# Optimization experiments

Measured on AMD Instinct MI355X. Metric: run time of the kernel, lower is better.

## Reference

```python
import jax, jax.numpy as jnp
import numpy as np

EPS = 1e-6

def _ln(x, g, b):
    mu = x.mean(-1, keepdims=True)
    var = ((x - mu) ** 2).mean(-1, keepdims=True)
    return (x - mu) * jax.lax.rsqrt(var + EPS) * g + b

def _ln_l2_grad(z, target, g, b):
    # grad of 0.5*||LN(z)*g+b - target||^2 wrt z (fused L2/LayerNorm backward used by TTT)
    d = z.shape[-1]
    mu = z.mean(-1, keepdims=True)
    var = ((z - mu) ** 2).mean(-1, keepdims=True)
    std = jnp.sqrt(var + EPS)
    zh = (z - mu) / std
    go = (zh * g + b) - target
    gxh = go * g
    return (d * gxh - gxh.sum(-1, keepdims=True) - zh * (gxh * zh).sum(-1, keepdims=True)) / (d * std)

def _forward(x, W_down, b_down, Wq, Wk, Wv, Wo, W1, b1, ttt_g, ttt_b,
             lr_w, lr_b, post_g, post_b, norm_g, norm_b, W_up, b_up):
    B, S, D = x.shape
    A = W_down.shape[1]
    H, hd, _ = W1.shape
    # adapter down projection + SiLU
    h = jax.nn.silu(x @ W_down + b_down)                      # [B,S,A]
    # TTT-Linear: q/k/v projections split into heads
    xq = (h @ Wq).reshape(B, S, H, hd)
    xk = (h @ Wk).reshape(B, S, H, hd)
    xv = (h @ Wv).reshape(B, S, H, hd)
    eta = jax.nn.sigmoid(h @ lr_w + lr_b) / hd                # [B,S,H] token-wise learnable inner lr (base_lr=1)
    W1_0 = jnp.broadcast_to(W1, (B, H, hd, hd))
    b1_0 = jnp.broadcast_to(b1, (B, H, 1, hd))
    xs = (xq.transpose(1, 0, 2, 3), xk.transpose(1, 0, 2, 3),
          xv.transpose(1, 0, 2, 3), eta.transpose(1, 0, 2))

    def step(carry, ins):
        W, bb = carry                                         # [B,H,hd,hd], [B,H,1,hd]
        q, k, v, e = ins                                      # [B,H,hd] x3, [B,H]
        Z = jnp.einsum('bhd,bhde->bhe', k, W) + bb[:, :, 0, :]
        g = _ln_l2_grad(Z, v - k, ttt_g, ttt_b)               # inner-loop grad wrt pre-LN activations
        e4 = e[:, :, None, None]
        Wn = W - e4 * (k[..., :, None] * g[..., None, :])     # fast-weight SGD update
        bn = bb - e4 * g[:, :, None, :]
        Zq = jnp.einsum('bhd,bhde->bhe', q, Wn) + bn[:, :, 0, :]
        out = q + _ln(Zq, ttt_g, ttt_b)                       # per-head TTT post residual
        return (Wn, bn), out

    _, ys = jax.lax.scan(step, (W1_0, b1_0), xs)              # ys: [S,B,H,hd]
    t = ys.transpose(1, 0, 2, 3).reshape(B, S, A)
    t = _ln(t, post_g, post_b) @ Wo                           # TTT post-norm + output projection
    out = _ln(t, norm_g, norm_b)                              # adapter LayerNorm
    return out @ W_up + b_up                                  # adapter up projection (residual unused in source)

def setup_inputs() -> dict:
    key = jax.random.key(0)
    ks = jax.random.split(key, 12)
    B, S, D, A, H = 4, 1024, 768, 192, 3
    hd = A // H
    s = 0.02
    return {
        'x': jax.random.normal(ks[0], (B, S, D), jnp.float32),
        'W_down': jax.random.normal(ks[1], (D, A), jnp.float32) * s,
        'b_down': jnp.zeros((A,), jnp.float32),
        'Wq': jax.random.normal(ks[2], (A, A), jnp.float32) * s,
        'Wk': jax.random.normal(ks[3], (A, A), jnp.float32) * s,
        'Wv': jax.random.normal(ks[4], (A, A), jnp.float32) * s,
        'Wo': jax.random.normal(ks[5], (A, A), jnp.float32) * s,
        'W1': jax.random.normal(ks[6], (H, hd, hd), jnp.float32) * s,
        'b1': jnp.zeros((H, 1, hd), jnp.float32),
        'ttt_g': jnp.ones((H, hd), jnp.float32),
        'ttt_b': jnp.zeros((H, hd), jnp.float32),
        'lr_w': jax.random.normal(ks[7], (A, H), jnp.float32) * s,
        'lr_b': jnp.zeros((H,), jnp.float32),
        'post_g': jnp.ones((A,), jnp.float32),
        'post_b': jnp.zeros((A,), jnp.float32),
        'norm_g': jnp.ones((A,), jnp.float32),
        'norm_b': jnp.zeros((A,), jnp.float32),
        'W_up': jax.random.normal(ks[8], (A, D), jnp.float32) * s,
        'b_up': jnp.zeros((D,), jnp.float32),
    }

def reference(x, W_down, b_down, Wq, Wk, Wv, Wo, W1, b1, ttt_g, ttt_b,
              lr_w, lr_b, post_g, post_b, norm_g, norm_b, W_up, b_up):
    return _forward(x, W_down, b_down, Wq, Wk, Wv, Wo, W1, b1, ttt_g, ttt_b,
                    lr_w, lr_b, post_g, post_b, norm_g, norm_b, W_up, b_up)
```

## Files before the change

### kernel.cpp

```cpp
#include <hip/hip_runtime.h>
#include <hip/hip_bf16.h>
#include <math.h>

#define BDIM 4
#define SDIM 1024
#define DDIM 768
#define ADIM 192
#define HDIM 3
#define HD   64
#define MROWS (BDIM*SDIM)
#define NCHUNK (SDIM/32)
#define EPSLN 1e-6f

template<int CTRL, int RMASK, bool BC>
__device__ __forceinline__ float dpp_add_step(float x) {
    int t = __builtin_amdgcn_update_dpp(0, __float_as_int(x), CTRL, RMASK, 0xf, BC);
    return x + __int_as_float(t);
}
__device__ __forceinline__ float wave_bcast_sum(float x) {
    x = dpp_add_step<0x111, 0xf, true >(x);
    x = dpp_add_step<0x112, 0xf, true >(x);
    x = dpp_add_step<0x114, 0xf, true >(x);
    x = dpp_add_step<0x118, 0xf, true >(x);
    x = dpp_add_step<0x142, 0xa, false>(x);
    x = dpp_add_step<0x143, 0xc, false>(x);
    return __int_as_float(__builtin_amdgcn_readlane(__float_as_int(x), 63));
}
__device__ __forceinline__ float rl(float v, int lane) {
    return __int_as_float(__builtin_amdgcn_readlane(__float_as_int(v), lane));
}
__device__ __forceinline__ float fast_rsq(float x) {
    float r;
    asm("v_rsq_f32 %0, %1" : "=v"(r) : "v"(x));
    return r;
}
__device__ __forceinline__ void red5_asm(float& a, float& b, float& c,
                                         float& d, float& e) {
#define R5_SHR(N)                                                              \
    asm("v_add_f32 %0, %0, %0 row_shr:" #N " row_mask:0xf bank_mask:0xf bound_ctrl:0" : "+v"(a)); \
    asm("v_add_f32 %0, %0, %0 row_shr:" #N " row_mask:0xf bank_mask:0xf bound_ctrl:0" : "+v"(b)); \
    asm("v_add_f32 %0, %0, %0 row_shr:" #N " row_mask:0xf bank_mask:0xf bound_ctrl:0" : "+v"(c)); \
    asm("v_add_f32 %0, %0, %0 row_shr:" #N " row_mask:0xf bank_mask:0xf bound_ctrl:0" : "+v"(d)); \
    asm("v_add_f32 %0, %0, %0 row_shr:" #N " row_mask:0xf bank_mask:0xf bound_ctrl:0" : "+v"(e));
#define R5_BC(N, RM)                                                           \
    asm("v_add_f32 %0, %0, %0 row_bcast:" #N " row_mask:" #RM " bank_mask:0xf" : "+v"(a)); \
    asm("v_add_f32 %0, %0, %0 row_bcast:" #N " row_mask:" #RM " bank_mask:0xf" : "+v"(b)); \
    asm("v_add_f32 %0, %0, %0 row_bcast:" #N " row_mask:" #RM " bank_mask:0xf" : "+v"(c)); \
    asm("v_add_f32 %0, %0, %0 row_bcast:" #N " row_mask:" #RM " bank_mask:0xf" : "+v"(d)); \
    asm("v_add_f32 %0, %0, %0 row_bcast:" #N " row_mask:" #RM " bank_mask:0xf" : "+v"(e));
    R5_SHR(1) R5_SHR(2) R5_SHR(4) R5_SHR(8)
    R5_BC(15, 0xa) R5_BC(31, 0xc)
#undef R5_SHR
#undef R5_BC
}

__global__ __launch_bounds__(64) void lnstats(
    const float* __restrict__ in, float2* __restrict__ st)
{
    int row = blockIdx.x, tid = threadIdx.x;
    float x0 = in[(size_t)row * ADIM + tid];
    float x1 = in[(size_t)row * ADIM + 64 + tid];
    float x2 = in[(size_t)row * ADIM + 128 + tid];
    float s1 = wave_bcast_sum((x0 + x1) + x2);
    float s2 = wave_bcast_sum(fmaf(x0, x0, fmaf(x1, x1, x2 * x2)));
    if (tid == 0) {
        float mu = s1 * (1.f / 192.f);
        float var = s2 * (1.f / 192.f) - mu * mu;
        st[row] = make_float2(mu, rsqrtf(var + EPSLN));
    }
}

template<int ACT, int LAYOUT, int LNA>
__global__ __launch_bounds__(256) void gemm_k(
    const float* __restrict__ A, const float* __restrict__ Bm,
    const float* __restrict__ bias, float* __restrict__ C,
    int M, int N, int K,
    const float2* __restrict__ lnst, const float* __restrict__ lng,
    const float* __restrict__ lnbb)
{
    __shared__ float As[16][68];
    __shared__ float Bs[16][68];
    const int tid = threadIdx.x;
    const int bm = blockIdx.y * 64, bn = blockIdx.x * 64;
    const int tr = tid >> 4, tc = tid & 15;
    float acc[4][4] = {};

    for (int k0 = 0; k0 < K; k0 += 16) {
        #pragma unroll
        for (int p = 0; p < 4; ++p) {
            int m = (tid >> 4) + p * 16;
            int kk = tid & 15;
            float av = A[(size_t)(bm + m) * K + k0 + kk];
            if (LNA) {
                float2 stv = lnst[bm + m];
                av = fmaf((av - stv.x) * stv.y, lng[k0 + kk], lnbb[k0 + kk]);
            }
            As[kk][m] = av;
        }
        #pragma unroll
        for (int p = 0; p < 4; ++p) {
            int kk = (tid >> 6) + p * 4;
            int n = tid & 63;
            Bs[kk][n] = Bm[(size_t)(k0 + kk) * N + bn + n];
        }
        __syncthreads();
        #pragma unroll
        for (int kk = 0; kk < 16; ++kk) {
            const float4 a4 = *(const float4*)&As[kk][tr * 4];
            const float4 b4 = *(const float4*)&Bs[kk][tc * 4];
            float aa[4] = {a4.x, a4.y, a4.z, a4.w};
            float bb[4] = {b4.x, b4.y, b4.z, b4.w};
            #pragma unroll
            for (int i = 0; i < 4; ++i)
                #pragma unroll
                for (int j = 0; j < 4; ++j)
                    acc[i][j] = fmaf(aa[i], bb[j], acc[i][j]);
        }
        __syncthreads();
    }

    #pragma unroll
    for (int i = 0; i < 4; ++i) {
        int m = bm + tr * 4 + i;
        #pragma unroll
        for (int j = 0; j < 4; ++j) {
            int n = bn + tc * 4 + j;
            float v = acc[i][j];
            if (bias) v += bias[n];
            if (ACT == 1) v = v / (1.f + __expf(-v));
            if (LAYOUT == 0) {
                C[(size_t)m * N + n] = v;
            } else {
                int b  = m >> 10, s = m & 1023;
                int hh = n >> 6,  d = n & 63;
                C[(((size_t)b * HDIM + hh) * SDIM + s) * HD + d] = v;
            }
        }
    }
}

__global__ __launch_bounds__(256) void gemm_qkv(
    const float* __restrict__ A, const float* __restrict__ BWq,
    const float* __restrict__ BWk, const float* __restrict__ BWv,
    float* __restrict__ Cbase)
{
    const float* Bm = (blockIdx.z == 0) ? BWq : (blockIdx.z == 1) ? BWk : BWv;
    float* C = Cbase + (size_t)blockIdx.z * ((size_t)MROWS * ADIM);
    __shared__ float As[16][68];
    __shared__ float Bs[16][68];
    const int tid = threadIdx.x;
    const int bm = blockIdx.y * 64, bn = blockIdx.x * 64;
    const int tr = tid >> 4, tc = tid & 15;
    float acc[4][4] = {};

    for (int k0 = 0; k0 < ADIM; k0 += 16) {
        #pragma unroll
        for (int p = 0; p < 4; ++p) {
            int m = (tid >> 4) + p * 16;
            int kk = tid & 15;
            As[kk][m] = A[(size_t)(bm + m) * ADIM + k0 + kk];
        }
        #pragma unroll
        for (int p = 0; p < 4; ++p) {
            int kk = (tid >> 6) + p * 4;
            int n = tid & 63;
            Bs[kk][n] = Bm[(size_t)(k0 + kk) * ADIM + bn + n];
        }
        __syncthreads();
        #pragma unroll
        for (int kk = 0; kk < 16; ++kk) {
            const float4 a4 = *(const float4*)&As[kk][tr * 4];
            const float4 b4 = *(const float4*)&Bs[kk][tc * 4];
            float aa[4] = {a4.x, a4.y, a4.z, a4.w};
            float bb[4] = {b4.x, b4.y, b4.z, b4.w};
            #pragma unroll
            for (int i = 0; i < 4; ++i)
                #pragma unroll
                for (int j = 0; j < 4; ++j)
                    acc[i][j] = fmaf(aa[i], bb[j], acc[i][j]);
        }
        __syncthreads();
    }

    #pragma unroll
    for (int i = 0; i < 4; ++i) {
        int m = bm + tr * 4 + i;
        #pragma unroll
        for (int j = 0; j < 4; ++j) {
            int n = bn + tc * 4 + j;
            int b  = m >> 10, s = m & 1023;
            int hh = n >> 6,  d = n & 63;
            C[(((size_t)b * HDIM + hh) * SDIM + s) * HD + d] = acc[i][j];
        }
    }
}

__global__ __launch_bounds__(192) void eta_kernel(
    const float* __restrict__ h, const float* __restrict__ lr_w,
    const float* __restrict__ lr_b, float* __restrict__ etab)
{
    const int row = blockIdx.x, tid = threadIdx.x, wave = tid >> 6;
    __shared__ float part[3][3];
    float hv = h[(size_t)row * ADIM + tid];
    float p0 = hv * lr_w[tid * 3 + 0];
    float p1 = hv * lr_w[tid * 3 + 1];
    float p2 = hv * lr_w[tid * 3 + 2];
    float s0 = wave_bcast_sum(p0);
    float s1 = wave_bcast_sum(p1);
    float s2 = wave_bcast_sum(p2);
    if ((tid & 63) == 0) {
        part[wave][0] = s0; part[wave][1] = s1; part[wave][2] = s2;
    }
    __syncthreads();
    if (tid < 3) {
        float acc = (part[0][tid] + part[1][tid]) + part[2][tid] + lr_b[tid];
        float e = 1.f / (1.f + __expf(-acc)) * (1.f / 64.f);
        int b = row >> 10, s = row & 1023;
        etab[((size_t)(b * HDIM + tid)) * SDIM + s] = e;
    }
}

__global__ __launch_bounds__(256) void ab_kernel(
    const float* __restrict__ qb, const float* __restrict__ kb,
    float* __restrict__ vb,
    const float* __restrict__ ttt_g, const float* __restrict__ ttt_b,
    float* __restrict__ Ab, float* __restrict__ Bb,
    float* __restrict__ r6b)
{
    int bh = blockIdx.x >> 5, c = blockIdx.x & 31, cs = c * 32;
    int hh = bh % HDIM;
    __shared__ float Kc[32][65], Qc[32][65], Vc[32][65];
    for (int i = threadIdx.x; i < 2048; i += 256) {
        int t = i >> 6, j = i & 63;
        Kc[t][j] = kb[((size_t)bh * SDIM + cs + t) * HD + j];
        Qc[t][j] = qb[((size_t)bh * SDIM + cs + t) * HD + j];
        Vc[t][j] = vb[((size_t)bh * SDIM + cs + t) * HD + j];
    }
    __syncthreads();
    size_t base = ((size_t)(bh * NCHUNK + c)) * 1024;
    for (int e = threadIdx.x; e < 1024; e += 256) {
        int t = e >> 5, s = e & 31;
        float a = 1.f, b = 1.f;
        #pragma unroll
        for (int j = 0; j < 64; ++j) {
            float ks = Kc[s][j];
            a = fmaf(Kc[t][j], ks, a);
            b = fmaf(Qc[t][j], ks, b);
        }
        Ab[base + e] = a;
        Bb[base + e] = b;
    }
    for (int i = threadIdx.x; i < 2048; i += 256) {
        int t = i >> 6, j = i & 63;
        float gwv = ttt_g[hh * 64 + j], bwv = ttt_b[hh * 64 + j];
        float av = fmaf(-(Vc[t][j] - Kc[t][j]), gwv, bwv * gwv);
        Vc[t][j] = av;
        vb[((size_t)bh * SDIM + cs + t) * HD + j] = av;
    }
    __syncthreads();
    if (threadIdx.x < 32) {
        int t = threadIdx.x;
        float acc = 0.f;
        #pragma unroll
        for (int j = 0; j < 64; ++j) acc += Vc[t][j];
        r6b[(size_t)bh * SDIM + cs + t] = acc;
    }
}

__device__ __forceinline__ void stage_chunk(
    int pp, int cc, int bh, int idx, int nth,
    const float* __restrict__ kbuf, const float* __restrict__ abuf,
    const float* __restrict__ Ab, const float* __restrict__ etab,
    const float* __restrict__ r6b,
    float4* K4, float4* a4, float4* A4, float2* er6)
{
    const float4* kg = (const float4*)(kbuf + ((size_t)bh * SDIM + cc * 32) * HD);
    const float4* ag = (const float4*)(abuf + ((size_t)bh * SDIM + cc * 32) * HD);
    const float4* Ag = (const float4*)(Ab + ((size_t)(bh * NCHUNK + cc)) * 1024);
    for (int i = idx; i < 512; i += nth) K4[pp * 512 + i] = kg[i];
    for (int i = idx; i < 512; i += nth) a4[pp * 512 + i] = ag[i];
    for (int i = idx; i < 256; i += nth) A4[pp * 256 + i] = Ag[i];
    for (int i = idx; i < 32; i += nth)
        er6[pp * 32 + i] = make_float2(
            etab[(size_t)bh * SDIM + cc * 32 + i] * (1.f / 64.f),
            r6b[(size_t)bh * SDIM + cc * 32 + i]);
}

__global__ __launch_bounds__(256, 1) void ttt_scan(
    const float* __restrict__ kbuf, const float* __restrict__ abuf,
    const float* __restrict__ etab, const float* __restrict__ Ab,
    const float* __restrict__ r6b,
    const float* __restrict__ W1,   const float* __restrict__ b1,
    const float* __restrict__ ttt_g, const float* __restrict__ ttt_b,
    float* __restrict__ Gbuf, float* __restrict__ W0save, float* __restrict__ b0save)
{
    const int bh = blockIdx.x, hh = bh % HDIM;
    const int tid = threadIdx.x, lane = tid & 63;
    const int wv = tid >> 6;
    __shared__ float  Zp[4][16][64];
    __shared__ float4 K4s[2 * 512];
    __shared__ float4 a4s[2 * 512];
    __shared__ float4 A4s[2 * 256];
    __shared__ float2 er6s[2 * 32];
    __shared__ float  Gl[16][64];

    float Wreg[16];
    #pragma unroll
    for (int r = 0; r < 16; ++r)
        Wreg[r] = W1[hh * 4096 + (wv * 16 + r) * 64 + lane];
    float breg = b1[hh * 64 + lane];
    const float gw = ttt_g[hh * 64 + lane];
    const float bw = ttt_b[hh * 64 + lane];
    const float w3 = gw * gw;
    (void)bw;
    const float Cg2 = wave_bcast_sum(w3);
    const float* a_f = (const float*)a4s;

    stage_chunk(0, 0, bh, tid, 256, kbuf, abuf, Ab, etab, r6b,
                K4s, a4s, A4s, er6s);
    __syncthreads();

    for (int c = 0; c < NCHUNK; ++c) {
        const int cs = c * 32;
        const int p = c & 1;

        {
            float* Wd = W0save + ((size_t)(bh * NCHUNK + c)) * 4096
                        + (wv * 16) * 64 + lane;
            #pragma unroll
            for (int r = 0; r < 16; ++r) Wd[r * 64] = Wreg[r];
            if (tid < 64) b0save[(bh * NCHUNK + c) * 64 + tid] = breg;
        }

        #pragma unroll
        for (int h = 0; h < 2; ++h) {
            const int h16 = h * 16, h4 = h * 4;

            float Zt[16];
            #pragma unroll
            for (int i = 0; i < 16; ++i) {
                const int t = h16 + i;
                float zt = 0.f;
                #pragma unroll
                for (int r4 = 0; r4 < 4; ++r4) {
                    const float4 kv = K4s[p * 512 + t * 16 + wv * 4 + r4];
                    zt = fmaf(kv.x, Wreg[r4 * 4 + 0], zt);
                    zt = fmaf(kv.y, Wreg[r4 * 4 + 1], zt);
                    zt = fmaf(kv.z, Wreg[r4 * 4 + 2], zt);
                    zt = fmaf(kv.w, Wreg[r4 * 4 + 3], zt);
                }
                Zt[i] = zt;
            }
            if (wv != 0) {
                #pragma unroll
                for (int i = 0; i < 16; ++i) Zp[wv][i][lane] = Zt[i];
            }
            __syncthreads();

            if (wv == 0) {
                float Z[16];
                #pragma unroll
                for (int i = 0; i < 16; ++i) {
                    float q1 = Zp[1][i][lane], q2 = Zp[2][i][lane],
                          q3 = Zp[3][i][lane];
                    Z[i] = ((Zt[i] + q1) + (q2 + q3)) + breg;
                }
                float4 avA[4], avB[4];
                float aA, aB; float2 erA, erB;
                #pragma unroll
                for (int q = 0; q < 4; ++q)
                    avA[q] = A4s[p * 256 + h16 * 8 + h4 + q];
                aA  = a_f[p * 2048 + h16 * 64 + lane];
                erA = er6s[p * 32 + h16];
#define TOK(I, avC, aC, erC, avN, aN, erN)                                     \
    {                                                                          \
        if ((I) < 15) {                                                        \
            _Pragma("unroll")                                                  \
            for (int q = 0; q < 4; ++q)                                        \
                avN[q] = A4s[p * 256 + (h16 + (I) + 1) * 8 + h4 + q];          \
            aN  = a_f[p * 2048 + (h16 + (I) + 1) * 64 + lane];                 \
            erN = er6s[p * 32 + h16 + (I) + 1];                                \
        }                                                                      \
        float z  = Z[I];                                                       \
        float a  = aC;                                                         \
        float zg = z * w3;                                                     \
        float x1 = z, x2 = z * z, x3 = zg, x4 = zg * z, x5 = z * a;            \
        red5_asm(x1, x2, x3, x4, x5);                                          \
        float r1 = rl(x1, 63), r2 = rl(x2, 63), r3 = rl(x3, 63);               \
        float r4 = rl(x4, 63), r5 = rl(x5, 63);                                \
        float r6t = (erC).y;                                                   \
        float mu   = r1 * (1.f / 64.f);                                        \
        float var  = fmaf(-mu, mu, r2 * (1.f / 64.f));                         \
        float rstd = fast_rsq(var + EPSLN);                                    \
        float mc   = mu * Cg2;                                                 \
        float sgxh = fmaf(rstd, r3 - mc, r6t);                                 \
        float t4v  = fmaf(mu, mc, fmaf(-2.f * mu, r3, r4));                    \
        float sgz  = fmaf(rstd * rstd, t4v, rstd * (r5 - mu * r6t));           \
        float zh   = (z - mu) * rstd;                                          \
        float gxh  = fmaf(zh, w3, a);                                          \
        float ge   = (fmaf(64.f, gxh, -sgxh) - zh * sgz) * (rstd * (erC).x);   \
        Gl[I][lane] = ge;                                                      \
        _Pragma("unroll")                                                      \
        for (int u = (I) + 1; u < 16; ++u) {                                   \
            const float4 c4 = avC[(u) >> 2]; const int m4 = (u) & 3;           \
            float Atu = (m4 == 0) ? c4.x : (m4 == 1) ? c4.y                    \
                      : (m4 == 2) ? c4.z : c4.w;                               \
            Z[u] = fmaf(-Atu, ge, Z[u]);                                       \
        }                                                                      \
    }
                #pragma unroll
                for (int tp = 0; tp < 8; ++tp) {
                    TOK(2 * tp,     avA, aA, erA, avB, aB, erB)
                    TOK(2 * tp + 1, avB, aB, erB, avA, aA, erA)
                }
#undef TOK
            } else if (h == 0 && c < NCHUNK - 1) {
                stage_chunk(p ^ 1, c + 1, bh, tid - 64, 192,
                            kbuf, abuf, Ab, etab, r6b, K4s, a4s, A4s, er6s);
            }
            __syncthreads();

            float btot = 0.f;
            #pragma unroll
            for (int s = 0; s < 16; ++s) {
                float gd = Gl[s][lane];
                btot += gd;
                #pragma unroll
                for (int r4 = 0; r4 < 4; ++r4) {
                    const float4 kv = K4s[p * 512 + (h16 + s) * 16 + wv * 4 + r4];
                    Wreg[r4 * 4 + 0] = fmaf(-kv.x, gd, Wreg[r4 * 4 + 0]);
                    Wreg[r4 * 4 + 1] = fmaf(-kv.y, gd, Wreg[r4 * 4 + 1]);
                    Wreg[r4 * 4 + 2] = fmaf(-kv.z, gd, Wreg[r4 * 4 + 2]);
                    Wreg[r4 * 4 + 3] = fmaf(-kv.w, gd, Wreg[r4 * 4 + 3]);
                }
            }
            breg -= btot;
            {
                float* gb = Gbuf + ((size_t)bh * SDIM + cs + h16) * HD + lane;
                #pragma unroll
                for (int r = 0; r < 4; ++r)
                    gb[(wv * 4 + r) * HD] = Gl[wv * 4 + r][lane];
            }
        }
    }
}

__global__ __launch_bounds__(256) void post_kernel(
    const float* __restrict__ qbuf, const float* __restrict__ Bb,
    const float* __restrict__ Gbuf, const float* __restrict__ W0save,
    const float* __restrict__ b0save,
    const float* __restrict__ ttt_g, const float* __restrict__ ttt_b,
    float* __restrict__ ys)
{
    const int bh = blockIdx.x >> 5, c = blockIdx.x & 31, cs = c * 32;
    const int b = bh / HDIM, hh = bh % HDIM;
    const int tid = threadIdx.x, lane = tid & 63, wave = tid >> 6;
    __shared__ float Qc[32][65];
    __shared__ float W0l[64][65];
    __shared__ float Gl[32][64];
    for (int i = tid; i < 2048; i += 256) {
        int t = i >> 6, j = i & 63;
        Qc[t][j] = qbuf[((size_t)bh * SDIM + cs + t) * HD + j];
        Gl[t][j] = Gbuf[((size_t)bh * SDIM + cs + t) * HD + j];
    }
    for (int i = tid; i < 4096; i += 256)
        W0l[i >> 6][i & 63] = W0save[((size_t)(bh * NCHUNK + c)) * 4096 + i];
    __syncthreads();

    const float bb0 = b0save[(bh * NCHUNK + c) * 64 + lane];
    const float gw = ttt_g[hh * 64 + lane], bw = ttt_b[hh * 64 + lane];
    float acc[8];
    #pragma unroll
    for (int r = 0; r < 8; ++r) acc[r] = bb0;
    for (int j = 0; j < 64; ++j) {
        float w0 = W0l[j][lane];
        #pragma unroll
        for (int r = 0; r < 8; ++r)
            acc[r] = fmaf(Qc[wave * 8 + r][j], w0, acc[r]);
    }
    float Breg[8];
    size_t bbase = ((size_t)(bh * NCHUNK + c)) * 1024;
    #pragma unroll
    for (int r = 0; r < 8; ++r)
        Breg[r] = Bb[bbase + (wave * 8 + r) * 32 + (lane & 31)];
    #pragma unroll
    for (int s = 0; s < 32; ++s) {
        float gd = Gl[s][lane];
        #pragma unroll
        for (int r = 0; r < 8; ++r) {
            int t = wave * 8 + r;
            float Bts = rl(Breg[r], s);
            acc[r] = (s <= t) ? fmaf(-Bts, gd, acc[r]) : acc[r];
        }
    }
    #pragma unroll
    for (int r = 0; r < 8; ++r) {
        int t = wave * 8 + r;
        float s1 = wave_bcast_sum(acc[r]);
        float s2 = wave_bcast_sum(acc[r] * acc[r]);
        float mu = s1 * (1.f / 64.f);
        float var = s2 * (1.f / 64.f) - mu * mu;
        float rstd = rsqrtf(var + EPSLN);
        float zh = (acc[r] - mu) * rstd;
        float val = zh * gw + bw + Qc[t][lane];
        ys[((size_t)(b * SDIM) + cs + t) * ADIM + hh * HD + lane] = val;
    }
}

extern "C" void kernel_launch(void* const* d_in, const int* in_sizes, int n_in,
                              void* d_out, int out_size, void* d_ws, size_t ws_size,
                              hipStream_t stream)
{
    const float* x      = (const float*)d_in[0];
    const float* W_down = (const float*)d_in[1];
    const float* b_down = (const float*)d_in[2];
    const float* Wq     = (const float*)d_in[3];
    const float* Wk     = (const float*)d_in[4];
    const float* Wv     = (const float*)d_in[5];
    const float* Wo     = (const float*)d_in[6];
    const float* W1     = (const float*)d_in[7];
    const float* b1     = (const float*)d_in[8];
    const float* ttt_g  = (const float*)d_in[9];
    const float* ttt_b  = (const float*)d_in[10];
    const float* lr_w   = (const float*)d_in[11];
    const float* lr_b   = (const float*)d_in[12];
    const float* post_g = (const float*)d_in[13];
    const float* post_b = (const float*)d_in[14];
    const float* norm_g = (const float*)d_in[15];
    const float* norm_b = (const float*)d_in[16];
    const float* W_up   = (const float*)d_in[17];
    const float* b_up   = (const float*)d_in[18];
    float* out = (float*)d_out;

    float* ws = (float*)d_ws;
    const size_t SZ = (size_t)MROWS * ADIM;
    float* h    = ws;
    float* qb   = ws + SZ;
    float* kb   = ws + 2 * SZ;
    float* vb   = ws + 3 * SZ;
    float* Gb   = ws + 4 * SZ;
    float* etab = ws + 5 * SZ;
    float* Ab   = etab + 12288;
    float* Bb   = Ab + 393216;
    float* W0s  = Bb + 393216;
    float* b0s  = W0s + 1572864;
    float* r6b  = b0s + 24576;
    float2* lnst = (float2*)(r6b + 12288);
    float* ysb  = h;
    float* tbuf = qb;

    gemm_k<1, 0, 0><<<dim3(ADIM / 64, MROWS / 64), 256, 0, stream>>>(
        x, W_down, b_down, h, MROWS, ADIM, DDIM, nullptr, nullptr, nullptr);
    gemm_qkv<<<dim3(ADIM / 64, MROWS / 64, 3), 256, 0, stream>>>(
        h, Wq, Wk, Wv, qb);
    eta_kernel<<<MROWS, 192, 0, stream>>>(h, lr_w, lr_b, etab);
    ab_kernel<<<BDIM * HDIM * NCHUNK, 256, 0, stream>>>(
        qb, kb, vb, ttt_g, ttt_b, Ab, Bb, r6b);
    ttt_scan<<<BDIM * HDIM, 256, 0, stream>>>(
        kb, vb, etab, Ab, r6b, W1, b1, ttt_g, ttt_b, Gb, W0s, b0s);
    post_kernel<<<BDIM * HDIM * NCHUNK, 256, 0, stream>>>(
        qb, Bb, Gb, W0s, b0s, ttt_g, ttt_b, ysb);
    lnstats<<<MROWS, 64, 0, stream>>>(ysb, lnst);
    gemm_k<0, 0, 1><<<dim3(ADIM / 64, MROWS / 64), 256, 0, stream>>>(
        ysb, Wo, nullptr, tbuf, MROWS, ADIM, ADIM, lnst, post_g, post_b);
    lnstats<<<MROWS, 64, 0, stream>>>(tbuf, lnst);
    gemm_k<0, 0, 1><<<dim3(DDIM / 64, MROWS / 64), 256, 0, stream>>>(
        tbuf, W_up, b_up, out, MROWS, DDIM, ADIM, lnst, norm_g, norm_b);
}
```

Measured before the change: 458.9 us.

## Process full 32-token chunk per barrier in TTT scan, read eta/r6 packed from global

The sequential scan kernel now handles all 32 tokens of a chunk in one phase instead of two 16-token halves, halving the number of block barriers and W-update passes per chunk. Eta and the row sums are written interleaved as float2 by the producer kernels, with the 1/64 scaling folded into eta_kernel. Wave 0 now reads the a-values and eta pairs straight from global memory instead of from staged shared memory. This raises register pressure (32-entry Z and 8 float4 A rows), and wave 0's serial loop now depends on global load latency, which the one-token-ahead prefetch only partly hides.

```diff
diff --git a/kernel.cpp b/kernel.cpp
--- a/kernel.cpp
+++ b/kernel.cpp
@@ -197,7 +197,7 @@
 
 __global__ __launch_bounds__(192) void eta_kernel(
     const float* __restrict__ h, const float* __restrict__ lr_w,
-    const float* __restrict__ lr_b, float* __restrict__ etab)
+    const float* __restrict__ lr_b, float2* __restrict__ er6b)
 {
     const int row = blockIdx.x, tid = threadIdx.x, wave = tid >> 6;
     __shared__ float part[3][3];
@@ -214,9 +214,9 @@
     __syncthreads();
     if (tid < 3) {
         float acc = (part[0][tid] + part[1][tid]) + part[2][tid] + lr_b[tid];
-        float e = 1.f / (1.f + __expf(-acc)) * (1.f / 64.f);
+        float e = 1.f / (1.f + __expf(-acc)) * (1.f / 4096.f);
         int b = row >> 10, s = row & 1023;
-        etab[((size_t)(b * HDIM + tid)) * SDIM + s] = e;
+        er6b[(size_t)(b * HDIM + tid) * SDIM + s].x = e;
     }
 }
 
@@ -225,7 +225,7 @@
     float* __restrict__ vb,
     const float* __restrict__ ttt_g, const float* __restrict__ ttt_b,
     float* __restrict__ Ab, float* __restrict__ Bb,
-    float* __restrict__ r6b)
+    float2* __restrict__ er6b)
 {
     int bh = blockIdx.x >> 5, c = blockIdx.x & 31, cs = c * 32;
     int hh = bh % HDIM;
@@ -263,33 +263,24 @@
         float acc = 0.f;
         #pragma unroll
         for (int j = 0; j < 64; ++j) acc += Vc[t][j];
-        r6b[(size_t)bh * SDIM + cs + t] = acc;
+        er6b[(size_t)bh * SDIM + cs + t].y = acc;
     }
 }
 
 __device__ __forceinline__ void stage_chunk(
     int pp, int cc, int bh, int idx, int nth,
-    const float* __restrict__ kbuf, const float* __restrict__ abuf,
-    const float* __restrict__ Ab, const float* __restrict__ etab,
-    const float* __restrict__ r6b,
-    float4* K4, float4* a4, float4* A4, float2* er6)
+    const float* __restrict__ kbuf, const float* __restrict__ Ab,
+    float4* K4, float4* A4)
 {
     const float4* kg = (const float4*)(kbuf + ((size_t)bh * SDIM + cc * 32) * HD);
-    const float4* ag = (const float4*)(abuf + ((size_t)bh * SDIM + cc * 32) * HD);
     const float4* Ag = (const float4*)(Ab + ((size_t)(bh * NCHUNK + cc)) * 1024);
     for (int i = idx; i < 512; i += nth) K4[pp * 512 + i] = kg[i];
-    for (int i = idx; i < 512; i += nth) a4[pp * 512 + i] = ag[i];
     for (int i = idx; i < 256; i += nth) A4[pp * 256 + i] = Ag[i];
-    for (int i = idx; i < 32; i += nth)
-        er6[pp * 32 + i] = make_float2(
-            etab[(size_t)bh * SDIM + cc * 32 + i] * (1.f / 64.f),
-            r6b[(size_t)bh * SDIM + cc * 32 + i]);
 }
 
 __global__ __launch_bounds__(256, 1) void ttt_scan(
     const float* __restrict__ kbuf, const float* __restrict__ abuf,
-    const float* __restrict__ etab, const float* __restrict__ Ab,
-    const float* __restrict__ r6b,
+    const float2* __restrict__ er6b, const float* __restrict__ Ab,
     const float* __restrict__ W1,   const float* __restrict__ b1,
     const float* __restrict__ ttt_g, const float* __restrict__ ttt_b,
     float* __restrict__ Gbuf, float* __restrict__ W0save, float* __restrict__ b0save)
@@ -297,12 +288,10 @@
     const int bh = blockIdx.x, hh = bh % HDIM;
     const int tid = threadIdx.x, lane = tid & 63;
     const int wv = tid >> 6;
-    __shared__ float  Zp[4][16][64];
+    __shared__ float  Zp[3][32][64];
     __shared__ float4 K4s[2 * 512];
-    __shared__ float4 a4s[2 * 512];
     __shared__ float4 A4s[2 * 256];
-    __shared__ float2 er6s[2 * 32];
-    __shared__ float  Gl[16][64];
+    __shared__ float  Gl[32][64];
 
     float Wreg[16];
     #pragma unroll
@@ -314,10 +303,8 @@
     const float w3 = gw * gw;
     (void)bw;
     const float Cg2 = wave_bcast_sum(w3);
-    const float* a_f = (const float*)a4s;
-
-    stage_chunk(0, 0, bh, tid, 256, kbuf, abuf, Ab, etab, r6b,
-                K4s, a4s, A4s, er6s);
+
+    stage_chunk(0, 0, bh, tid, 256, kbuf, Ab, K4s, A4s);
     __syncthreads();
 
     for (int c = 0; c < NCHUNK; ++c) {
@@ -332,54 +319,45 @@
             if (tid < 64) b0save[(bh * NCHUNK + c) * 64 + tid] = breg;
         }
 
-        #pragma unroll
-        for (int h = 0; h < 2; ++h) {
-            const int h16 = h * 16, h4 = h * 4;
-
-            float Zt[16];
-            #pragma unroll
-            for (int i = 0; i < 16; ++i) {
-                const int t = h16 + i;
-                float zt = 0.f;
-                #pragma unroll
-                for (int r4 = 0; r4 < 4; ++r4) {
-                    const float4 kv = K4s[p * 512 + t * 16 + wv * 4 + r4];
-                    zt = fmaf(kv.x, Wreg[r4 * 4 + 0], zt);
-                    zt = fmaf(kv.y, Wreg[r4 * 4 + 1], zt);
-                    zt = fmaf(kv.z, Wreg[r4 * 4 + 2], zt);
-                    zt = fmaf(kv.w, Wreg[r4 * 4 + 3], zt);
-                }
-                Zt[i] = zt;
+        float Z[32];
+        #pragma unroll
+        for (int i = 0; i < 32; ++i) {
+            float zt = 0.f;
+            #pragma unroll
+            for (int r4 = 0; r4 < 4; ++r4) {
+                const float4 kv = K4s[p * 512 + i * 16 + wv * 4 + r4];
+                zt = fmaf(kv.x, Wreg[r4 * 4 + 0], zt);
+                zt = fmaf(kv.y, Wreg[r4 * 4 + 1], zt);
+                zt = fmaf(kv.z, Wreg[r4 * 4 + 2], zt);
+                zt = fmaf(kv.w, Wreg[r4 * 4 + 3], zt);
             }
-            if (wv != 0) {
-                #pragma unroll
-                for (int i = 0; i < 16; ++i) Zp[wv][i][lane] = Zt[i];
-            }
-            __syncthreads();
-
-            if (wv == 0) {
-                float Z[16];
-                #pragma unroll
-                for (int i = 0; i < 16; ++i) {
-                    float q1 = Zp[1][i][lane], q2 = Zp[2][i][lane],
-                          q3 = Zp[3][i][lane];
-                    Z[i] = ((Zt[i] + q1) + (q2 + q3)) + breg;
-                }
-                float4 avA[4], avB[4];
-                float aA, aB; float2 erA, erB;
-                #pragma unroll
-                for (int q = 0; q < 4; ++q)
-                    avA[q] = A4s[p * 256 + h16 * 8 + h4 + q];
-                aA  = a_f[p * 2048 + h16 * 64 + lane];
-                erA = er6s[p * 32 + h16];
+            if (wv != 0) Zp[wv - 1][i][lane] = zt;
+            else         Z[i] = zt;
+        }
+        __syncthreads();
+
+        if (wv == 0) {
+            const float*  ag = abuf + ((size_t)bh * SDIM + cs) * HD;
+            const float2* eg = er6b + (size_t)bh * SDIM + cs;
+            float  aA = ag[lane];
+            float2 erA = eg[0];
+            float  aB; float2 erB;
+            #pragma unroll
+            for (int i = 0; i < 32; ++i)
+                Z[i] = ((Z[i] + Zp[0][i][lane]) +
+                        (Zp[1][i][lane] + Zp[2][i][lane])) + breg;
+            float4 avA[8], avB[8];
+            #pragma unroll
+            for (int q = 0; q < 8; ++q)
+                avA[q] = A4s[p * 256 + q];
 #define TOK(I, avC, aC, erC, avN, aN, erN)                                     \
     {                                                                          \
-        if ((I) < 15) {                                                        \
+        if ((I) < 31) {                                                        \
             _Pragma("unroll")                                                  \
-            for (int q = 0; q < 4; ++q)                                        \
-                avN[q] = A4s[p * 256 + (h16 + (I) + 1) * 8 + h4 + q];          \
-            aN  = a_f[p * 2048 + (h16 + (I) + 1) * 64 + lane];                 \
-            erN = er6s[p * 32 + h16 + (I) + 1];                                \
+            for (int q = 0; q < 8; ++q)                                        \
+                avN[q] = A4s[p * 256 + ((I) + 1) * 8 + q];                     \
+            aN  = ag[((I) + 1) * HD + lane];                                   \
+            erN = eg[(I) + 1];                                                 \
         }                                                                      \
         float z  = Z[I];                                                       \
         float a  = aC;                                                         \
@@ -401,46 +379,44 @@
         float ge   = (fmaf(64.f, gxh, -sgxh) - zh * sgz) * (rstd * (erC).x);   \
         Gl[I][lane] = ge;                                                      \
         _Pragma("unroll")                                                      \
-        for (int u = (I) + 1; u < 16; ++u) {                                   \
+        for (int u = (I) + 1; u < 32; ++u) {                                   \
             const float4 c4 = avC[(u) >> 2]; const int m4 = (u) & 3;           \
             float Atu = (m4 == 0) ? c4.x : (m4 == 1) ? c4.y                    \
                       : (m4 == 2) ? c4.z : c4.w;                               \
             Z[u] = fmaf(-Atu, ge, Z[u]);                                       \
         }                                                                      \
     }
-                #pragma unroll
-                for (int tp = 0; tp < 8; ++tp) {
-                    TOK(2 * tp,     avA, aA, erA, avB, aB, erB)
-                    TOK(2 * tp + 1, avB, aB, erB, avA, aA, erA)
-                }
+            #pragma unroll
+            for (int tp = 0; tp < 16; ++tp) {
+                TOK(2 * tp,     avA, aA, erA, avB, aB, erB)
+                TOK(2 * tp + 1, avB, aB, erB, avA, aA, erA)
+            }
 #undef TOK
-            } else if (h == 0 && c < NCHUNK - 1) {
-                stage_chunk(p ^ 1, c + 1, bh, tid - 64, 192,
-                            kbuf, abuf, Ab, etab, r6b, K4s, a4s, A4s, er6s);
+        } else if (c < NCHUNK - 1) {
+            stage_chunk(p ^ 1, c + 1, bh, tid - 64, 192, kbuf, Ab, K4s, A4s);
+        }
+        __syncthreads();
+
+        float btot = 0.f;
+        #pragma unroll
+        for (int s = 0; s < 32; ++s) {
+            float gd = Gl[s][lane];
+            btot += gd;
+            #pragma unroll
+            for (int r4 = 0; r4 < 4; ++r4) {
+                const float4 kv = K4s[p * 512 + s * 16 + wv * 4 + r4];
+                Wreg[r4 * 4 + 0] = fmaf(-kv.x, gd, Wreg[r4 * 4 + 0]);
+                Wreg[r4 * 4 + 1] = fmaf(-kv.y, gd, Wreg[r4 * 4 + 1]);
+                Wreg[r4 * 4 + 2] = fmaf(-kv.z, gd, Wreg[r4 * 4 + 2]);
+                Wreg[r4 * 4 + 3] = fmaf(-kv.w, gd, Wreg[r4 * 4 + 3]);
             }
-            __syncthreads();
-
-            float btot = 0.f;
-            #pragma unroll
-            for (int s = 0; s < 16; ++s) {
-                float gd = Gl[s][lane];
-                btot += gd;
-                #pragma unroll
-                for (int r4 = 0; r4 < 4; ++r4) {
-                    const float4 kv = K4s[p * 512 + (h16 + s) * 16 + wv * 4 + r4];
-                    Wreg[r4 * 4 + 0] = fmaf(-kv.x, gd, Wreg[r4 * 4 + 0]);
-                    Wreg[r4 * 4 + 1] = fmaf(-kv.y, gd, Wreg[r4 * 4 + 1]);
-                    Wreg[r4 * 4 + 2] = fmaf(-kv.z, gd, Wreg[r4 * 4 + 2]);
-                    Wreg[r4 * 4 + 3] = fmaf(-kv.w, gd, Wreg[r4 * 4 + 3]);
-                }
-            }
-            breg -= btot;
-            {
-                float* gb = Gbuf + ((size_t)bh * SDIM + cs + h16) * HD + lane;
-                #pragma unroll
-                for (int r = 0; r < 4; ++r)
-                    gb[(wv * 4 + r) * HD] = Gl[wv * 4 + r][lane];
-            }
+        }
+        breg -= btot;
+        {
+            float* gb = Gbuf + ((size_t)bh * SDIM + cs) * HD + lane;
+            #pragma unroll
+            for (int r = 0; r < 8; ++r)
+                gb[(wv * 8 + r) * HD] = Gl[wv * 8 + r][lane];
         }
     }
 }
@@ -539,13 +515,12 @@
     float* kb   = ws + 2 * SZ;
     float* vb   = ws + 3 * SZ;
     float* Gb   = ws + 4 * SZ;
-    float* etab = ws + 5 * SZ;
-    float* Ab   = etab + 12288;
+    float2* er6b = (float2*)(ws + 5 * SZ);
+    float* Ab   = ws + 5 * SZ + 24576;
     float* Bb   = Ab + 393216;
     float* W0s  = Bb + 393216;
     float* b0s  = W0s + 1572864;
-    float* r6b  = b0s + 24576;
-    float2* lnst = (float2*)(r6b + 12288);
+    float2* lnst = (float2*)(b0s + 24576);
     float* ysb  = h;
     float* tbuf = qb;
 
@@ -553,11 +528,11 @@
         x, W_down, b_down, h, MROWS, ADIM, DDIM, nullptr, nullptr, nullptr);
     gemm_qkv<<<dim3(ADIM / 64, MROWS / 64, 3), 256, 0, stream>>>(
         h, Wq, Wk, Wv, qb);
-    eta_kernel<<<MROWS, 192, 0, stream>>>(h, lr_w, lr_b, etab);
+    eta_kernel<<<MROWS, 192, 0, stream>>>(h, lr_w, lr_b, er6b);
     ab_kernel<<<BDIM * HDIM * NCHUNK, 256, 0, stream>>>(
-        qb, kb, vb, ttt_g, ttt_b, Ab, Bb, r6b);
+        qb, kb, vb, ttt_g, ttt_b, Ab, Bb, er6b);
     ttt_scan<<<BDIM * HDIM, 256, 0, stream>>>(
-        kb, vb, etab, Ab, r6b, W1, b1, ttt_g, ttt_b, Gb, W0s, b0s);
+        kb, vb, er6b, Ab, W1, b1, ttt_g, ttt_b, Gb, W0s, b0s);
     post_kernel<<<BDIM * HDIM * NCHUNK, 256, 0, stream>>>(
         qb, Bb, Gb, W0s, b0s, ttt_g, ttt_b, ysb);
     lnstats<<<MROWS, 64, 0, stream>>>(ysb, lnst);
```

Result: slower. 580.8 us (+26.6%).
